# Optimization experiments

Hardware: AMD Instinct MI355X
Metric: run time of the kernel (lower is better)

Reference implementation:

```python
import jax, jax.numpy as jnp
import numpy as np
import math

T_MIN = 0.1
T_MAX = 1.0


def setup_inputs() -> dict:
    key = jax.random.key(0)
    k1, k2, k3, k4, k5, k6 = jax.random.split(key, 6)
    B, H, SQ, SK, DK = 1, 16, 4096, 4096, 64
    query = jax.random.normal(k1, (B, H, SQ, DK), dtype=jnp.float32)
    key_t = jax.random.normal(k2, (B, H, SK, DK), dtype=jnp.float32)
    # MLP params (3 -> 16 -> 1). Original zero-inits the last layer; we use
    # small random values so gradients flow to query/key in the bwd test.
    W1 = jax.random.normal(k3, (16, 3), dtype=jnp.float32) * 0.5
    b1 = jax.random.normal(k4, (16,), dtype=jnp.float32) * 0.1
    W2 = jax.random.normal(k5, (1, 16), dtype=jnp.float32) * 0.5
    b2 = jax.random.normal(k6, (1,), dtype=jnp.float32) * 0.1
    return {"query": query, "key": key_t, "W1": W1, "b1": b1, "W2": W2, "b2": b2}


def reference(query, key, W1, b1, W2, b2):
    d_k = query.shape[-1]
    sk = key.shape[-2]
    q = query.astype(jnp.float32)
    k = key.astype(jnp.float32)
    # [B,H,Sq,Sk] score matrix
    scores = jnp.einsum('bhqd,bhkd->bhqk', q, k) / math.sqrt(d_k)
    scores = jnp.clip(scores, -50.0, 50.0)
    mean_sim = scores.mean(axis=(-2, -1))                 # [B,H]
    max_sim = scores.max(axis=-1).mean(axis=-1)           # [B,H]
    probs = jax.nn.softmax(scores / 2.0, axis=-1)         # [B,H,Sq,Sk]
    # torch .var(dim=-1) is unbiased (divisor Sk-1)
    pm = probs.mean(axis=-1, keepdims=True)
    var = ((probs - pm) ** 2).sum(axis=-1) / (sk - 1)     # [B,H,Sq]
    entropy_proxy = var.mean(axis=-1)                     # [B,H]
    mean_sim = jnp.clip(mean_sim, -10.0, 10.0)
    max_sim = jnp.clip(max_sim, -10.0, 10.0)
    entropy_proxy = jnp.clip(entropy_proxy, 0.0, 1.0)
    features = jnp.stack([mean_sim, max_sim, entropy_proxy], axis=-1)  # [B,H,3]
    h = jnp.tanh(features @ W1.T + b1)
    raw_t = h @ W2.T + b2                                 # [B,H,1]
    t = T_MIN + jax.nn.sigmoid(raw_t) * (T_MAX - T_MIN)
    t = jnp.clip(t, T_MIN, T_MAX)
    return t[..., None].astype(query.dtype)               # [B,H,1,1]
```

## Files before the change

kernel.cpp:

```cpp
#include <hip/hip_runtime.h>
#include <math.h>

#define NH   16
#define SQL  4096
#define SKL  4096
#define DK   64
#define QB   128
#define KB   128
#define NKT  (SKL / KB)

#define QSCALE  0.090168440f
#define UNSCALE 1.3862943611f

typedef __bf16 bf16x8 __attribute__((ext_vector_type(8)));
typedef __bf16 bf16x4 __attribute__((ext_vector_type(4)));
typedef float  f32x4  __attribute__((ext_vector_type(4)));
typedef float  f32x2  __attribute__((ext_vector_type(2)));

#if __has_builtin(__builtin_amdgcn_exp2f)
#define EXP2(x) __builtin_amdgcn_exp2f(x)
#else
#define EXP2(x) exp2f(x)
#endif

static __device__ __forceinline__ f32x2 pk_fma(f32x2 a, f32x2 b, f32x2 c) {
#if __has_builtin(__builtin_elementwise_fma)
    return __builtin_elementwise_fma(a, b, c);
#else
    f32x2 r; r[0] = fmaf(a[0], b[0], c[0]); r[1] = fmaf(a[1], b[1], c[1]); return r;
#endif
}
static __device__ __forceinline__ f32x2 pk_max(f32x2 a, f32x2 b) {
#if __has_builtin(__builtin_elementwise_max)
    return __builtin_elementwise_max(a, b);
#else
    f32x2 r; r[0] = fmaxf(a[0], b[0]); r[1] = fmaxf(a[1], b[1]); return r;
#endif
}

__device__ __forceinline__ int swz(int row, int col_bytes) {
    return ((row << 7) + col_bytes) ^ ((row & 7) << 4);
}

__global__ __launch_bounds__(512, 4) void dtp_stats_mfma(const float* __restrict__ Q,
                                                         const float* __restrict__ K,
                                                         float* __restrict__ partial) {
    __shared__ __align__(16) unsigned char Qs[QB * DK * 2];
    __shared__ __align__(16) unsigned char Ks[2][KB * DK * 2];
    __shared__ float red[32][3];

    const int qb   = blockIdx.x;
    const int h    = blockIdx.y;
    const int tid  = threadIdx.x;
    const int lane = tid & 63;
    const int w    = tid >> 6;
    const int l15  = lane & 15;
    const int lg   = lane >> 4;

    const float* Qh = Q + ((size_t)h * SQL + (size_t)qb * QB) * DK;
    const float* Kh = K + (size_t)h * SKL * DK;

    const int sc4 = tid & 15;
    const int sr0 = tid >> 4;

    #pragma unroll
    for (int j = 0; j < 4; ++j) {
        int r = sr0 + 32 * j;
        const float4 v = *reinterpret_cast<const float4*>(Qh + r * DK + sc4 * 4);
        bf16x4 hv;
        hv[0] = (__bf16)(v.x * QSCALE); hv[1] = (__bf16)(v.y * QSCALE);
        hv[2] = (__bf16)(v.z * QSCALE); hv[3] = (__bf16)(v.w * QSCALE);
        *reinterpret_cast<bf16x4*>(&Qs[swz(r, sc4 * 8)]) = hv;
    }

    float4 kreg[4];
    #pragma unroll
    for (int j = 0; j < 4; ++j)
        kreg[j] = *reinterpret_cast<const float4*>(Kh + (size_t)(sr0 + 32 * j) * DK + sc4 * 4);
    #pragma unroll
    for (int j = 0; j < 4; ++j) {
        int r = sr0 + 32 * j;
        bf16x4 hv;
        hv[0] = (__bf16)kreg[j].x; hv[1] = (__bf16)kreg[j].y;
        hv[2] = (__bf16)kreg[j].z; hv[3] = (__bf16)kreg[j].w;
        *reinterpret_cast<bf16x4*>(&Ks[0][swz(r, sc4 * 8)]) = hv;
    }
    #pragma unroll
    for (int j = 0; j < 4; ++j)
        kreg[j] = *reinterpret_cast<const float4*>(Kh + (size_t)(KB + sr0 + 32 * j) * DK + sc4 * 4);

    __syncthreads();

    bf16x8 aF[2];
    {
        int r = w * 16 + l15;
        aF[0] = *reinterpret_cast<const bf16x8*>(&Qs[swz(r, 0 * 64 + lg * 16)]);
        aF[1] = *reinterpret_cast<const bf16x8*>(&Qs[swz(r, 1 * 64 + lg * 16)]);
    }

    f32x2 rsum01 = {0.f, 0.f}, rsum23 = {0.f, 0.f};
    f32x2 rmx01  = {-3.0e38f, -3.0e38f}, rmx23 = {-3.0e38f, -3.0e38f};
    f32x2 rs1_01 = {0.f, 0.f}, rs1_23 = {0.f, 0.f};
    f32x2 rs2_01 = {0.f, 0.f}, rs2_23 = {0.f, 0.f};

    for (int kt = 0; kt < NKT; ++kt) {
        const int cur = kt & 1;

        if (kt + 1 < NKT) {
            #pragma unroll
            for (int j = 0; j < 4; ++j) {
                int r = sr0 + 32 * j;
                bf16x4 hv;
                hv[0] = (__bf16)kreg[j].x; hv[1] = (__bf16)kreg[j].y;
                hv[2] = (__bf16)kreg[j].z; hv[3] = (__bf16)kreg[j].w;
                *reinterpret_cast<bf16x4*>(&Ks[cur ^ 1][swz(r, sc4 * 8)]) = hv;
            }
            if (kt + 2 < NKT) {
                const float* Kt = Kh + (size_t)(kt + 2) * KB * DK;
                #pragma unroll
                for (int j = 0; j < 4; ++j)
                    kreg[j] = *reinterpret_cast<const float4*>(Kt + (size_t)(sr0 + 32 * j) * DK + sc4 * 4);
            }
        }

        f32x4 acc[8];
        #pragma unroll
        for (int ct = 0; ct < 8; ++ct) {
            int rr = ct * 16 + l15;
            bf16x8 b0 = *reinterpret_cast<const bf16x8*>(&Ks[cur][swz(rr, 0 * 64 + lg * 16)]);
            bf16x8 b1 = *reinterpret_cast<const bf16x8*>(&Ks[cur][swz(rr, 1 * 64 + lg * 16)]);
            f32x4 a = {0.f, 0.f, 0.f, 0.f};
            a = __builtin_amdgcn_mfma_f32_16x16x32_bf16(aF[0], b0, a, 0, 0, 0);
            a = __builtin_amdgcn_mfma_f32_16x16x32_bf16(aF[1], b1, a, 0, 0, 0);
            acc[ct] = a;
        }

        f32x2 s01 = {0.f, 0.f}, s23 = {0.f, 0.f};
        #pragma unroll
        for (int ct = 0; ct < 8; ++ct) {
            f32x2 v01 = __builtin_shufflevector(acc[ct], acc[ct], 0, 1);
            f32x2 v23 = __builtin_shufflevector(acc[ct], acc[ct], 2, 3);
            s01 += v01; s23 += v23;
            rmx01 = pk_max(rmx01, v01);
            rmx23 = pk_max(rmx23, v23);
            f32x2 e01, e23;
            e01[0] = EXP2(v01[0]); e01[1] = EXP2(v01[1]);
            e23[0] = EXP2(v23[0]); e23[1] = EXP2(v23[1]);
            rs1_01 += e01; rs1_23 += e23;
            rs2_01 = pk_fma(e01, e01, rs2_01);
            rs2_23 = pk_fma(e23, e23, rs2_23);
        }
        rsum01 += s01; rsum23 += s23;

        __syncthreads();
    }

    #pragma unroll
    for (int m = 1; m < 16; m <<= 1) {
        #pragma unroll
        for (int c = 0; c < 2; ++c) {
            rsum01[c] += __shfl_xor(rsum01[c], m, 64);
            rsum23[c] += __shfl_xor(rsum23[c], m, 64);
            rmx01[c]   = fmaxf(rmx01[c], __shfl_xor(rmx01[c], m, 64));
            rmx23[c]   = fmaxf(rmx23[c], __shfl_xor(rmx23[c], m, 64));
            rs1_01[c] += __shfl_xor(rs1_01[c], m, 64);
            rs1_23[c] += __shfl_xor(rs1_23[c], m, 64);
            rs2_01[c] += __shfl_xor(rs2_01[c], m, 64);
            rs2_23[c] += __shfl_xor(rs2_23[c], m, 64);
        }
    }

    if (l15 == 0) {
        float bs = (rsum01[0] + rsum01[1]) + (rsum23[0] + rsum23[1]);
        float bm = (rmx01[0] + rmx01[1]) + (rmx23[0] + rmx23[1]);
        float bv = 0.f;
        const float invSK = 1.0f / (float)SKL, invSK1 = 1.0f / (float)(SKL - 1);
        {
            float r1[4] = {rs1_01[0], rs1_01[1], rs1_23[0], rs1_23[1]};
            float r2[4] = {rs2_01[0], rs2_01[1], rs2_23[0], rs2_23[1]};
            #pragma unroll
            for (int i = 0; i < 4; ++i)
                bv += (r2[i] / (r1[i] * r1[i]) - invSK) * invSK1;
        }
        red[w * 4 + lg][0] = bs * UNSCALE;
        red[w * 4 + lg][1] = bm * UNSCALE;
        red[w * 4 + lg][2] = bv;
    }
    __syncthreads();
    if (tid == 0) {
        float bs = 0.f, bm = 0.f, bv = 0.f;
        #pragma unroll
        for (int i = 0; i < 32; ++i) { bs += red[i][0]; bm += red[i][1]; bv += red[i][2]; }
        float* p = partial + (size_t)(h * 32 + qb) * 3;
        p[0] = bs; p[1] = bm; p[2] = bv;
    }
}

__global__ __launch_bounds__(64) void dtp_finalize_kernel(const float* __restrict__ partial,
                                                          const float* __restrict__ W1,
                                                          const float* __restrict__ b1,
                                                          const float* __restrict__ W2,
                                                          const float* __restrict__ b2,
                                                          float* __restrict__ out) {
    int h = threadIdx.x;
    if (h >= NH) return;
    float ssum = 0.f, smax = 0.f, svar = 0.f;
    for (int qb = 0; qb < 32; ++qb) {
        const float* p = partial + (size_t)(h * 32 + qb) * 3;
        ssum += p[0]; smax += p[1]; svar += p[2];
    }
    float mean_sim = ssum / ((float)SQL * (float)SKL);
    float max_sim  = smax / (float)SQL;
    float entropy  = svar / (float)SQL;
    mean_sim = fminf(fmaxf(mean_sim, -10.f), 10.f);
    max_sim  = fminf(fmaxf(max_sim,  -10.f), 10.f);
    entropy  = fminf(fmaxf(entropy,    0.f), 1.f);
    float raw = b2[0];
    #pragma unroll
    for (int i = 0; i < 16; ++i) {
        float a = b1[i] + W1[i*3+0] * mean_sim + W1[i*3+1] * max_sim + W1[i*3+2] * entropy;
        raw += W2[i] * tanhf(a);
    }
    float t = 0.1f + 0.9f / (1.0f + __expf(-raw));
    t = fminf(fmaxf(t, 0.1f), 1.0f);
    out[h] = t;
}

extern "C" void kernel_launch(void* const* d_in, const int* in_sizes, int n_in,
                              void* d_out, int out_size, void* d_ws, size_t ws_size,
                              hipStream_t stream) {
    const float* Q  = (const float*)d_in[0];
    const float* K  = (const float*)d_in[1];
    const float* W1 = (const float*)d_in[2];
    const float* b1 = (const float*)d_in[3];
    const float* W2 = (const float*)d_in[4];
    const float* b2 = (const float*)d_in[5];
    float* out      = (float*)d_out;
    float* partial  = (float*)d_ws;

    dim3 grid(SQL / QB, NH);
    dtp_stats_mfma<<<grid, 512, 0, stream>>>(Q, K, partial);
    dtp_finalize_kernel<<<1, 64, 0, stream>>>(partial, W1, b1, W2, b2, out);
}
```

Baseline: 75.70 us.

## Split key dimension across two blocks and merge per-row stats in finalize

Adds a third grid dimension that splits the key sequence into two halves, so each block processes half the keys with 64-row K tiles, doubling the block count. Per-row max, exp-sum and exp-squared-sum are written to workspace, and a new parallel finalize kernel (one block per head) merges the halves and computes the variance proxy. The intent is better GPU occupancy and load balance from 512 to 1024 blocks, with higher launch_bounds occupancy. The cost is redundant Q loads and conversion per block, more workspace traffic, and a heavier finalize step.

```diff
diff --git a/kernel.cpp b/kernel.cpp
--- a/kernel.cpp
+++ b/kernel.cpp
@@ -6,11 +6,16 @@
 #define SKL  4096
 #define DK   64
 #define QB   128
-#define KB   128
-#define NKT  (SKL / KB)
+#define KB   64
+#define KSPLIT 2
+#define KHALF (SKL / KSPLIT)
+#define NKT   (KHALF / KB)
 
 #define QSCALE  0.090168440f
 #define UNSCALE 1.3862943611f
+
+#define NB2      (NH * 32 * KSPLIT)
+#define ROWFLOAT (NB2 * QB)
 
 typedef __bf16 bf16x8 __attribute__((ext_vector_type(8)));
 typedef __bf16 bf16x4 __attribute__((ext_vector_type(4)));
@@ -42,15 +47,19 @@
     return ((row << 7) + col_bytes) ^ ((row & 7) << 4);
 }
 
-__global__ __launch_bounds__(512, 4) void dtp_stats_mfma(const float* __restrict__ Q,
+__global__ __launch_bounds__(512, 8) void dtp_stats_mfma(const float* __restrict__ Q,
                                                          const float* __restrict__ K,
-                                                         float* __restrict__ partial) {
+                                                         float* __restrict__ RSUM,
+                                                         float* __restrict__ RMX,
+                                                         float* __restrict__ RS1,
+                                                         float* __restrict__ RS2) {
     __shared__ __align__(16) unsigned char Qs[QB * DK * 2];
     __shared__ __align__(16) unsigned char Ks[2][KB * DK * 2];
-    __shared__ float red[32][3];
+    __shared__ float red[32];
 
     const int qb   = blockIdx.x;
     const int h    = blockIdx.y;
+    const int half = blockIdx.z;
     const int tid  = threadIdx.x;
     const int lane = tid & 63;
     const int w    = tid >> 6;
@@ -58,7 +67,7 @@
     const int lg   = lane >> 4;
 
     const float* Qh = Q + ((size_t)h * SQL + (size_t)qb * QB) * DK;
-    const float* Kh = K + (size_t)h * SKL * DK;
+    const float* Kh = K + ((size_t)h * SKL + (size_t)half * KHALF) * DK;
 
     const int sc4 = tid & 15;
     const int sr0 = tid >> 4;
@@ -73,12 +82,12 @@
         *reinterpret_cast<bf16x4*>(&Qs[swz(r, sc4 * 8)]) = hv;
     }
 
-    float4 kreg[4];
-    #pragma unroll
-    for (int j = 0; j < 4; ++j)
+    float4 kreg[2];
+    #pragma unroll
+    for (int j = 0; j < 2; ++j)
         kreg[j] = *reinterpret_cast<const float4*>(Kh + (size_t)(sr0 + 32 * j) * DK + sc4 * 4);
     #pragma unroll
-    for (int j = 0; j < 4; ++j) {
+    for (int j = 0; j < 2; ++j) {
         int r = sr0 + 32 * j;
         bf16x4 hv;
         hv[0] = (__bf16)kreg[j].x; hv[1] = (__bf16)kreg[j].y;
@@ -86,7 +95,7 @@
         *reinterpret_cast<bf16x4*>(&Ks[0][swz(r, sc4 * 8)]) = hv;
     }
     #pragma unroll
-    for (int j = 0; j < 4; ++j)
+    for (int j = 0; j < 2; ++j)
         kreg[j] = *reinterpret_cast<const float4*>(Kh + (size_t)(KB + sr0 + 32 * j) * DK + sc4 * 4);
 
     __syncthreads();
@@ -108,7 +117,7 @@
 
         if (kt + 1 < NKT) {
             #pragma unroll
-            for (int j = 0; j < 4; ++j) {
+            for (int j = 0; j < 2; ++j) {
                 int r = sr0 + 32 * j;
                 bf16x4 hv;
                 hv[0] = (__bf16)kreg[j].x; hv[1] = (__bf16)kreg[j].y;
@@ -118,14 +127,14 @@
             if (kt + 2 < NKT) {
                 const float* Kt = Kh + (size_t)(kt + 2) * KB * DK;
                 #pragma unroll
-                for (int j = 0; j < 4; ++j)
+                for (int j = 0; j < 2; ++j)
                     kreg[j] = *reinterpret_cast<const float4*>(Kt + (size_t)(sr0 + 32 * j) * DK + sc4 * 4);
             }
         }
 
-        f32x4 acc[8];
-        #pragma unroll
-        for (int ct = 0; ct < 8; ++ct) {
+        f32x4 acc[4];
+        #pragma unroll
+        for (int ct = 0; ct < 4; ++ct) {
             int rr = ct * 16 + l15;
             bf16x8 b0 = *reinterpret_cast<const bf16x8*>(&Ks[cur][swz(rr, 0 * 64 + lg * 16)]);
             bf16x8 b1 = *reinterpret_cast<const bf16x8*>(&Ks[cur][swz(rr, 1 * 64 + lg * 16)]);
@@ -135,12 +144,11 @@
             acc[ct] = a;
         }
 
-        f32x2 s01 = {0.f, 0.f}, s23 = {0.f, 0.f};
-        #pragma unroll
-        for (int ct = 0; ct < 8; ++ct) {
+        #pragma unroll
+        for (int ct = 0; ct < 4; ++ct) {
             f32x2 v01 = __builtin_shufflevector(acc[ct], acc[ct], 0, 1);
             f32x2 v23 = __builtin_shufflevector(acc[ct], acc[ct], 2, 3);
-            s01 += v01; s23 += v23;
+            rsum01 += v01; rsum23 += v23;
             rmx01 = pk_max(rmx01, v01);
             rmx23 = pk_max(rmx23, v23);
             f32x2 e01, e23;
@@ -150,7 +158,6 @@
             rs2_01 = pk_fma(e01, e01, rs2_01);
             rs2_23 = pk_fma(e23, e23, rs2_23);
         }
-        rsum01 += s01; rsum23 += s23;
 
         __syncthreads();
     }
@@ -170,60 +177,90 @@
         }
     }
 
+    const int base = (h * 32 + qb) * KSPLIT + half;
     if (l15 == 0) {
-        float bs = (rsum01[0] + rsum01[1]) + (rsum23[0] + rsum23[1]);
-        float bm = (rmx01[0] + rmx01[1]) + (rmx23[0] + rmx23[1]);
-        float bv = 0.f;
-        const float invSK = 1.0f / (float)SKL, invSK1 = 1.0f / (float)(SKL - 1);
-        {
-            float r1[4] = {rs1_01[0], rs1_01[1], rs1_23[0], rs1_23[1]};
-            float r2[4] = {rs2_01[0], rs2_01[1], rs2_23[0], rs2_23[1]};
-            #pragma unroll
-            for (int i = 0; i < 4; ++i)
-                bv += (r2[i] / (r1[i] * r1[i]) - invSK) * invSK1;
-        }
-        red[w * 4 + lg][0] = bs * UNSCALE;
-        red[w * 4 + lg][1] = bm * UNSCALE;
-        red[w * 4 + lg][2] = bv;
+        const size_t rb = (size_t)base * QB + (w * 16 + lg * 4);
+        float4 mx = {rmx01[0] * UNSCALE, rmx01[1] * UNSCALE,
+                     rmx23[0] * UNSCALE, rmx23[1] * UNSCALE};
+        float4 s1 = {rs1_01[0], rs1_01[1], rs1_23[0], rs1_23[1]};
+        float4 s2 = {rs2_01[0], rs2_01[1], rs2_23[0], rs2_23[1]};
+        *reinterpret_cast<float4*>(&RMX[rb]) = mx;
+        *reinterpret_cast<float4*>(&RS1[rb]) = s1;
+        *reinterpret_cast<float4*>(&RS2[rb]) = s2;
+        red[w * 4 + lg] = (rsum01[0] + rsum01[1]) + (rsum23[0] + rsum23[1]);
     }
     __syncthreads();
     if (tid == 0) {
-        float bs = 0.f, bm = 0.f, bv = 0.f;
-        #pragma unroll
-        for (int i = 0; i < 32; ++i) { bs += red[i][0]; bm += red[i][1]; bv += red[i][2]; }
-        float* p = partial + (size_t)(h * 32 + qb) * 3;
-        p[0] = bs; p[1] = bm; p[2] = bv;
-    }
-}
-
-__global__ __launch_bounds__(64) void dtp_finalize_kernel(const float* __restrict__ partial,
-                                                          const float* __restrict__ W1,
-                                                          const float* __restrict__ b1,
-                                                          const float* __restrict__ W2,
-                                                          const float* __restrict__ b2,
-                                                          float* __restrict__ out) {
-    int h = threadIdx.x;
-    if (h >= NH) return;
-    float ssum = 0.f, smax = 0.f, svar = 0.f;
-    for (int qb = 0; qb < 32; ++qb) {
-        const float* p = partial + (size_t)(h * 32 + qb) * 3;
-        ssum += p[0]; smax += p[1]; svar += p[2];
-    }
-    float mean_sim = ssum / ((float)SQL * (float)SKL);
-    float max_sim  = smax / (float)SQL;
-    float entropy  = svar / (float)SQL;
-    mean_sim = fminf(fmaxf(mean_sim, -10.f), 10.f);
-    max_sim  = fminf(fmaxf(max_sim,  -10.f), 10.f);
-    entropy  = fminf(fmaxf(entropy,    0.f), 1.f);
-    float raw = b2[0];
-    #pragma unroll
-    for (int i = 0; i < 16; ++i) {
-        float a = b1[i] + W1[i*3+0] * mean_sim + W1[i*3+1] * max_sim + W1[i*3+2] * entropy;
-        raw += W2[i] * tanhf(a);
-    }
-    float t = 0.1f + 0.9f / (1.0f + __expf(-raw));
-    t = fminf(fmaxf(t, 0.1f), 1.0f);
-    out[h] = t;
+        float bs = 0.f;
+        #pragma unroll
+        for (int i = 0; i < 32; ++i) bs += red[i];
+        RSUM[base] = bs * UNSCALE;
+    }
+}
+
+__global__ __launch_bounds__(256) void dtp_finalize(const float* __restrict__ RSUM,
+                                                    const float* __restrict__ RMX,
+                                                    const float* __restrict__ RS1,
+                                                    const float* __restrict__ RS2,
+                                                    const float* __restrict__ W1,
+                                                    const float* __restrict__ b1,
+                                                    const float* __restrict__ W2,
+                                                    const float* __restrict__ b2,
+                                                    float* __restrict__ out) {
+    const int h   = blockIdx.x;
+    const int tid = threadIdx.x;
+    const float invSK  = 1.0f / (float)SKL;
+    const float invSK1 = 1.0f / (float)(SKL - 1);
+
+    float sm = 0.f, sv = 0.f;
+    #pragma unroll
+    for (int j = 0; j < 16; ++j) {
+        int r  = tid + 256 * j;
+        int qb = r >> 7;
+        int rr = r & 127;
+        size_t b0 = ((size_t)(h * 32 + qb) * KSPLIT) * QB + rr;
+        size_t b1i = b0 + QB;
+        float mx = fmaxf(RMX[b0], RMX[b1i]);
+        float s1 = RS1[b0] + RS1[b1i];
+        float s2 = RS2[b0] + RS2[b1i];
+        sm += mx;
+        sv += (s2 / (s1 * s1) - invSK) * invSK1;
+    }
+
+    float ss = (tid < NH * 0 + 64) ? RSUM[h * 64 + (tid & 63)] : 0.f;
+    if (tid >= 64) ss = 0.f;
+
+    #pragma unroll
+    for (int m = 1; m < 64; m <<= 1) {
+        sm += __shfl_xor(sm, m, 64);
+        sv += __shfl_xor(sv, m, 64);
+        ss += __shfl_xor(ss, m, 64);
+    }
+    __shared__ float redm[4], redv[4], reds[4];
+    const int wv = tid >> 6;
+    if ((tid & 63) == 0) { redm[wv] = sm; redv[wv] = sv; reds[wv] = ss; }
+    __syncthreads();
+
+    if (tid == 0) {
+        float tsm = redm[0] + redm[1] + redm[2] + redm[3];
+        float tsv = redv[0] + redv[1] + redv[2] + redv[3];
+        float tss = reds[0];
+        float mean_sim = tss / ((float)SQL * (float)SKL);
+        float max_sim  = tsm / (float)SQL;
+        float entropy  = tsv / (float)SQL;
+        mean_sim = fminf(fmaxf(mean_sim, -10.f), 10.f);
+        max_sim  = fminf(fmaxf(max_sim,  -10.f), 10.f);
+        entropy  = fminf(fmaxf(entropy,    0.f), 1.f);
+        float raw = b2[0];
+        #pragma unroll
+        for (int i = 0; i < 16; ++i) {
+            float a = b1[i] + W1[i*3+0] * mean_sim + W1[i*3+1] * max_sim + W1[i*3+2] * entropy;
+            raw += W2[i] * tanhf(a);
+        }
+        float t = 0.1f + 0.9f / (1.0f + __expf(-raw));
+        t = fminf(fmaxf(t, 0.1f), 1.0f);
+        out[h] = t;
+    }
 }
 
 extern "C" void kernel_launch(void* const* d_in, const int* in_sizes, int n_in,
@@ -236,9 +273,13 @@
     const float* W2 = (const float*)d_in[4];
     const float* b2 = (const float*)d_in[5];
     float* out      = (float*)d_out;
-    float* partial  = (float*)d_ws;
-
-    dim3 grid(SQL / QB, NH);
-    dtp_stats_mfma<<<grid, 512, 0, stream>>>(Q, K, partial);
-    dtp_finalize_kernel<<<1, 64, 0, stream>>>(partial, W1, b1, W2, b2, out);
-}
+
+    float* RSUM = (float*)d_ws;
+    float* RMX  = RSUM + NB2;
+    float* RS1  = RMX + ROWFLOAT;
+    float* RS2  = RS1 + ROWFLOAT;
+
+    dim3 grid(SQL / QB, NH, KSPLIT);
+    dtp_stats_mfma<<<grid, 512, 0, stream>>>(Q, K, RSUM, RMX, RS1, RS2);
+    dtp_finalize<<<NH, 256, 0, stream>>>(RSUM, RMX, RS1, RS2, W1, b1, W2, b2, out);
+}
```

After: 77.72 us. 2.7% more time.
